# Kernel optimization log

Measured on AMD Instinct MI355X. Metric: run time of the kernel, lower is better.

Reference implementation:

```python
import jax, jax.numpy as jnp
import numpy as np

DECAY = 0.8      # cfg.ema_decay
EPS = 1e-5       # cfg.eps


def setup_inputs() -> dict:
    key = jax.random.key(0)
    k1, k2 = jax.random.split(key)
    H, B, N, D = 8, 8, 2048, 64   # num_codebooks, batch, seq, code_dim
    C = 1024                      # num_codes
    x = jax.random.normal(k1, (H, B, N, D), dtype=jnp.float32)
    embed = jax.random.normal(k2, (H, C, D), dtype=jnp.float32)
    embed_avg = embed.copy()
    cluster_size = jnp.ones((H, C), dtype=jnp.float32)
    return {"x": x, "embed": embed, "embed_avg": embed_avg, "cluster_size": cluster_size}


def reference(x, embed, embed_avg, cluster_size):
    # x: [h, b, n, d], embed: [h, c, d]
    h, b, n, d = x.shape
    c = embed.shape[1]
    flatten = x.reshape(h, b * n, d)  # pack 'h * d'

    # negative squared euclidean distance: -||f - e||^2
    f_sq = jnp.sum(flatten * flatten, axis=-1, keepdims=True)          # [h, N, 1]
    e_sq = jnp.sum(embed * embed, axis=-1)[:, None, :]                  # [h, 1, c]
    cross = jnp.einsum('hnd,hcd->hnc', flatten, embed)                  # [h, N, c]
    dist = -(f_sq - 2.0 * cross + e_sq)                                 # [h, N, c]

    # gumbel_sample with stochastic=False, straight_through=False -> argmax + one_hot
    embed_ind_flat = jnp.argmax(dist, axis=-1)                          # [h, N]
    embed_onehot = jax.nn.one_hot(embed_ind_flat, c, dtype=x.dtype)     # [h, N, c]

    # quantize (training path): onehot @ embed
    quantize = jnp.einsum('hnc,hcd->hnd', embed_onehot, embed).reshape(h, b, n, d)
    embed_ind = embed_ind_flat.reshape(h, b, n)

    # EMA codebook updates (ema_update=True, affine_params=False)
    cs_new = cluster_size * DECAY + embed_onehot.sum(axis=1) * (1.0 - DECAY)      # [h, c]
    embed_sum = jnp.einsum('hnd,hnc->hcd', flatten, embed_onehot)                  # [h, c, d]
    ea_new = embed_avg * DECAY + embed_sum * (1.0 - DECAY)                         # [h, c, d]

    ntot = jnp.sum(cs_new, axis=-1, keepdims=True)                                 # [h, 1]
    cs_smooth = (cs_new + EPS) / (ntot + c * EPS) * ntot                           # laplace smoothing * n
    embed_norm = ea_new / cs_smooth[..., None]                                     # new embed

    dist_out = dist.reshape(h, b, n, c)
    return quantize, embed_ind, embed_onehot, dist_out, embed_norm, ea_new, cs_new
```

## Files before the change

### kernel.cpp

```cpp
#include <hip/hip_runtime.h>

#define DECAY 0.8f
#define EPS   1e-5f
#define HN    8
#define BB    8
#define NSEQ  2048
#define DD    64
#define CC    1024
#define NROW  (BB*NSEQ)

#define LS 128
#define XS(k,r) xs[(k)*LS + (r)]
#define ES(k,c) es[(k)*LS + (c)]

typedef float vf4 __attribute__((ext_vector_type(4)));

__global__ void sumsq_kernel(const float* __restrict__ x, const float* __restrict__ embed,
                             float* __restrict__ fsq, float* __restrict__ esq) {
    int tid = blockIdx.x * blockDim.x + threadIdx.x;
    const int totalF = HN * NROW;
    const int totalE = HN * CC;
    if (tid < totalF) {
        const float4* src = (const float4*)(x + (size_t)tid * DD);
        float s = 0.f;
        #pragma unroll
        for (int i = 0; i < DD/4; ++i) {
            float4 v = src[i];
            s = fmaf(v.x, v.x, s); s = fmaf(v.y, v.y, s);
            s = fmaf(v.z, v.z, s); s = fmaf(v.w, v.w, s);
        }
        fsq[tid] = s;
    } else if (tid < totalF + totalE) {
        int t = tid - totalF;
        const float4* src = (const float4*)(embed + (size_t)t * DD);
        float s = 0.f;
        #pragma unroll
        for (int i = 0; i < DD/4; ++i) {
            float4 v = src[i];
            s = fmaf(v.x, v.x, s); s = fmaf(v.y, v.y, s);
            s = fmaf(v.z, v.z, s); s = fmaf(v.w, v.w, s);
        }
        esq[t] = s;
    }
}

__global__ __launch_bounds__(256, 2)
void dist_fp32_kernel(const float* __restrict__ x, const float* __restrict__ embed,
                      const float* __restrict__ fsq, const float* __restrict__ esq,
                      float* __restrict__ out_q, float* __restrict__ out_i,
                      float* __restrict__ out_oh, float* __restrict__ out_d) {
    __shared__ float xs[64 * LS];
    __shared__ float es[64 * LS];

    const int h   = blockIdx.y;
    const int n0  = blockIdx.x * 128;
    const int tid = threadIdx.x;
    const int ty  = tid >> 4;
    const int tx  = tid & 15;

    const float* xh_   = x     + (size_t)h * NROW * DD;
    const float* eh_   = embed + (size_t)h * CC   * DD;
    const float* esq_h = esq   + h * CC;

    const int g4 = (tid & 31) * 4;
    const int k0 = (tid >> 5) * 8;

    {
        float4 v[2][4];
        #pragma unroll
        for (int t = 0; t < 2; ++t)
            #pragma unroll
            for (int i = 0; i < 4; ++i)
                v[t][i] = *(const float4*)(xh_ + (size_t)(n0 + g4 + i) * DD + k0 + t*4);
        #pragma unroll
        for (int t = 0; t < 2; ++t) {
            *(float4*)&XS(k0+t*4+0, g4) = make_float4(v[t][0].x, v[t][1].x, v[t][2].x, v[t][3].x);
            *(float4*)&XS(k0+t*4+1, g4) = make_float4(v[t][0].y, v[t][1].y, v[t][2].y, v[t][3].y);
            *(float4*)&XS(k0+t*4+2, g4) = make_float4(v[t][0].z, v[t][1].z, v[t][2].z, v[t][3].z);
            *(float4*)&XS(k0+t*4+3, g4) = make_float4(v[t][0].w, v[t][1].w, v[t][2].w, v[t][3].w);
        }
    }
    {
        float4 v[2][4];
        #pragma unroll
        for (int t = 0; t < 2; ++t)
            #pragma unroll
            for (int i = 0; i < 4; ++i)
                v[t][i] = *(const float4*)(eh_ + (size_t)(g4 + i) * DD + k0 + t*4);
        #pragma unroll
        for (int t = 0; t < 2; ++t) {
            *(float4*)&ES(k0+t*4+0, g4) = make_float4(v[t][0].x, v[t][1].x, v[t][2].x, v[t][3].x);
            *(float4*)&ES(k0+t*4+1, g4) = make_float4(v[t][0].y, v[t][1].y, v[t][2].y, v[t][3].y);
            *(float4*)&ES(k0+t*4+2, g4) = make_float4(v[t][0].z, v[t][1].z, v[t][2].z, v[t][3].z);
            *(float4*)&ES(k0+t*4+3, g4) = make_float4(v[t][0].w, v[t][1].w, v[t][2].w, v[t][3].w);
        }
    }
    asm volatile("s_waitcnt lgkmcnt(0)" ::: "memory");
    __builtin_amdgcn_s_barrier();

    float fs[8];
    #pragma unroll
    for (int i = 0; i < 8; ++i) fs[i] = fsq[h*NROW + n0 + ty*8 + i];

    float bestv[8];
    int   besti[8];
    #pragma unroll
    for (int i = 0; i < 8; ++i) { bestv[i] = -3.4e38f; besti[i] = 0; }

    #pragma unroll 1
    for (int ci = 0; ci < 8; ++ci) {
        const int c0 = ci * 128;

        float4 ev[2][4];
        if (ci < 7) {
            #pragma unroll
            for (int t = 0; t < 2; ++t)
                #pragma unroll
                for (int i = 0; i < 4; ++i)
                    ev[t][i] = *(const float4*)(eh_ + (size_t)(c0 + 128 + g4 + i) * DD + k0 + t*4);
        }

        float acc[8][8];
        #pragma unroll
        for (int i = 0; i < 8; ++i)
            #pragma unroll
            for (int j = 0; j < 8; ++j) acc[i][j] = 0.f;

        #pragma unroll 4
        for (int k = 0; k < 64; ++k) {
            float a[8], b[8];
            *(float4*)&a[0] = *(const float4*)&XS(k, ty*8);
            *(float4*)&a[4] = *(const float4*)&XS(k, ty*8 + 4);
            *(float4*)&b[0] = *(const float4*)&ES(k, tx*4);
            *(float4*)&b[4] = *(const float4*)&ES(k, 64 + tx*4);
            #pragma unroll
            for (int i = 0; i < 8; ++i)
                #pragma unroll
                for (int j = 0; j < 8; ++j)
                    acc[i][j] = fmaf(a[i], b[j], acc[i][j]);
        }

        float eq[8];
        *(float4*)&eq[0] = *(const float4*)(esq_h + c0 + tx*4);
        *(float4*)&eq[4] = *(const float4*)(esq_h + c0 + 64 + tx*4);

        #pragma unroll
        for (int i = 0; i < 8; ++i) {
            int row = n0 + ty*8 + i;
            float dv[8];
            #pragma unroll
            for (int j = 0; j < 8; ++j)
                dv[j] = fmaf(2.f, acc[i][j], -(fs[i] + eq[j]));

            size_t rb = ((size_t)h*NROW + row)*CC + c0;
            vf4 d0 = {dv[0], dv[1], dv[2], dv[3]};
            vf4 d1 = {dv[4], dv[5], dv[6], dv[7]};
            __builtin_nontemporal_store(d0, (vf4*)(out_d + rb + tx*4));
            __builtin_nontemporal_store(d1, (vf4*)(out_d + rb + 64 + tx*4));

            #pragma unroll
            for (int j = 0; j < 4; ++j) {
                if (dv[j] > bestv[i]) { bestv[i] = dv[j]; besti[i] = c0 + tx*4 + j; }
            }
            #pragma unroll
            for (int j = 4; j < 8; ++j) {
                if (dv[j] > bestv[i]) { bestv[i] = dv[j]; besti[i] = c0 + 64 + tx*4 + (j-4); }
            }
        }

        if (ci < 7) {
            asm volatile("s_waitcnt lgkmcnt(0)" ::: "memory");
            __builtin_amdgcn_s_barrier();
            #pragma unroll
            for (int t = 0; t < 2; ++t) {
                *(float4*)&ES(k0+t*4+0, g4) = make_float4(ev[t][0].x, ev[t][1].x, ev[t][2].x, ev[t][3].x);
                *(float4*)&ES(k0+t*4+1, g4) = make_float4(ev[t][0].y, ev[t][1].y, ev[t][2].y, ev[t][3].y);
                *(float4*)&ES(k0+t*4+2, g4) = make_float4(ev[t][0].z, ev[t][1].z, ev[t][2].z, ev[t][3].z);
                *(float4*)&ES(k0+t*4+3, g4) = make_float4(ev[t][0].w, ev[t][1].w, ev[t][2].w, ev[t][3].w);
            }
            asm volatile("s_waitcnt lgkmcnt(0)" ::: "memory");
            __builtin_amdgcn_s_barrier();
        }
    }


    #pragma unroll
    for (int i = 0; i < 8; ++i) {
        float v  = bestv[i];
        int   id = besti[i];
        #pragma unroll
        for (int off = 8; off >= 1; off >>= 1) {
            float ov = __shfl_xor(v, off, 64);
            int   oi = __shfl_xor(id, off, 64);
            if (ov > v || (ov == v && oi < id)) { v = ov; id = oi; }
        }
        int row = n0 + ty*8 + i;
        float4 qv = *(const float4*)(eh_ + (size_t)id*DD + tx*4);
        *(float4*)(out_q + ((size_t)h*NROW + row)*DD + tx*4) = qv;
        if (tx == 0) {
            out_i[(size_t)h*NROW + row] = (float)id;
            out_oh[((size_t)h*NROW + row)*CC + id] = 1.0f;
        }
    }
}

__global__ __launch_bounds__(64)
void ema_kernel(const float* __restrict__ x, const float* __restrict__ embed_avg,
                const float* __restrict__ cluster_size, const float* __restrict__ ind_f,
                float* __restrict__ out_cs, float* __restrict__ out_ea,
                float* __restrict__ out_norm) {
    const int h    = blockIdx.y;
    const int c    = blockIdx.x;
    const int lane = threadIdx.x;

    const float* cs_h = cluster_size + h*CC;
    float s = 0.f;
    #pragma unroll
    for (int i = 0; i < CC/64; ++i) s += cs_h[lane + i*64];
    #pragma unroll
    for (int off = 32; off >= 1; off >>= 1) s += __shfl_xor(s, off, 64);

    const float* xh   = x     + (size_t)h * NROW * DD;
    const float* indh = ind_f + (size_t)h * NROW;

    float sum_d = 0.f;
    int   cnt   = 0;
    for (int chunk = 0; chunk < NROW/64; ++chunk) {
        int myidx = (int)indh[chunk*64 + lane];
        unsigned long long m = __ballot(myidx == c);
        while (m) {
            int t = __ffsll(m) - 1;
            m &= m - 1;
            int n = chunk*64 + t;
            sum_d += xh[(size_t)n*DD + lane];
            cnt++;
        }
    }

    float csn  = cs_h[c]*DECAY + (float)cnt*(1.f - DECAY);
    float ea   = embed_avg[((size_t)h*CC + c)*DD + lane]*DECAY + sum_d*(1.f - DECAY);
    float ntot = s*DECAY + (1.f - DECAY)*(float)NROW;
    float css  = (csn + EPS) / (ntot + (float)CC*EPS) * ntot;

    out_ea  [((size_t)h*CC + c)*DD + lane] = ea;
    out_norm[((size_t)h*CC + c)*DD + lane] = ea / css;
    if (lane == 0) out_cs[h*CC + c] = csn;
}

extern "C" void kernel_launch(void* const* d_in, const int* in_sizes, int n_in,
                              void* d_out, int out_size, void* d_ws, size_t ws_size,
                              hipStream_t stream) {
    const float* x            = (const float*)d_in[0];
    const float* embed        = (const float*)d_in[1];
    const float* embed_avg    = (const float*)d_in[2];
    const float* cluster_size = (const float*)d_in[3];

    float* out = (float*)d_out;
    float* fsq = (float*)d_ws;
    float* esq = fsq + (size_t)HN * NROW;

    float* out_q    = out;
    float* out_i    = out_q    + (size_t)HN * NROW * DD;
    float* out_oh   = out_i    + (size_t)HN * NROW;
    float* out_d    = out_oh   + (size_t)HN * NROW * CC;
    float* out_norm = out_d    + (size_t)HN * NROW * CC;
    float* out_ea   = out_norm + (size_t)HN * CC * DD;
    float* out_cs   = out_ea   + (size_t)HN * CC * DD;

    hipMemsetAsync(out_oh, 0, (size_t)HN * NROW * CC * sizeof(float), stream);

    {
        int total = HN*NROW + HN*CC;
        sumsq_kernel<<<(total + 255)/256, 256, 0, stream>>>(x, embed, fsq, esq);
    }
    {
        dim3 g(NROW/128, HN);
        dist_fp32_kernel<<<g, 256, 0, stream>>>(x, embed, fsq, esq,
                                                out_q, out_i, out_oh, out_d);
    }
    {
        dim3 g(CC, HN);
        ema_kernel<<<g, 64, 0, stream>>>(x, embed_avg, cluster_size, out_i,
                                         out_cs, out_ea, out_norm);
    }
}
```

Baseline: 540.8 us.

## Halve embed LDS tile into K-halves to fit three blocks per CU

The embed shared-memory tile is split into two 32-deep K halves that are streamed in sequence, which halves the LDS footprint and cuts the prefetch registers from eight float4 to four. Launch bounds are raised from 2 to 3 blocks per SM so more blocks can be resident to hide the heavy distance-matrix store traffic. The cost is twice as many barriers per codebook chunk and a tighter register budget, which could cause spills with the 64-entry accumulator.

```diff
diff --git a/kernel.cpp b/kernel.cpp
--- a/kernel.cpp
+++ b/kernel.cpp
@@ -15,6 +15,9 @@
 
 typedef float vf4 __attribute__((ext_vector_type(4)));
 
+#define LGKM0_BAR() do { asm volatile("s_waitcnt lgkmcnt(0)" ::: "memory"); \
+                         __builtin_amdgcn_s_barrier(); } while (0)
+
 __global__ void sumsq_kernel(const float* __restrict__ x, const float* __restrict__ embed,
                              float* __restrict__ fsq, float* __restrict__ esq) {
     int tid = blockIdx.x * blockDim.x + threadIdx.x;
@@ -44,13 +47,13 @@
     }
 }
 
-__global__ __launch_bounds__(256, 2)
+__global__ __launch_bounds__(256, 3)
 void dist_fp32_kernel(const float* __restrict__ x, const float* __restrict__ embed,
                       const float* __restrict__ fsq, const float* __restrict__ esq,
                       float* __restrict__ out_q, float* __restrict__ out_i,
                       float* __restrict__ out_oh, float* __restrict__ out_d) {
     __shared__ float xs[64 * LS];
-    __shared__ float es[64 * LS];
+    __shared__ float es[32 * LS];
 
     const int h   = blockIdx.y;
     const int n0  = blockIdx.x * 128;
@@ -62,8 +65,9 @@
     const float* eh_   = embed + (size_t)h * CC   * DD;
     const float* esq_h = esq   + h * CC;
 
-    const int g4 = (tid & 31) * 4;
-    const int k0 = (tid >> 5) * 8;
+    const int g4  = (tid & 31) * 4;
+    const int k0x = (tid >> 5) * 8;
+    const int k0  = (tid >> 5) * 4;
 
     {
         float4 v[2][4];
@@ -71,32 +75,22 @@
         for (int t = 0; t < 2; ++t)
             #pragma unroll
             for (int i = 0; i < 4; ++i)
-                v[t][i] = *(const float4*)(xh_ + (size_t)(n0 + g4 + i) * DD + k0 + t*4);
+                v[t][i] = *(const float4*)(xh_ + (size_t)(n0 + g4 + i) * DD + k0x + t*4);
         #pragma unroll
         for (int t = 0; t < 2; ++t) {
-            *(float4*)&XS(k0+t*4+0, g4) = make_float4(v[t][0].x, v[t][1].x, v[t][2].x, v[t][3].x);
-            *(float4*)&XS(k0+t*4+1, g4) = make_float4(v[t][0].y, v[t][1].y, v[t][2].y, v[t][3].y);
-            *(float4*)&XS(k0+t*4+2, g4) = make_float4(v[t][0].z, v[t][1].z, v[t][2].z, v[t][3].z);
-            *(float4*)&XS(k0+t*4+3, g4) = make_float4(v[t][0].w, v[t][1].w, v[t][2].w, v[t][3].w);
-        }
-    }
-    {
-        float4 v[2][4];
-        #pragma unroll
-        for (int t = 0; t < 2; ++t)
-            #pragma unroll
-            for (int i = 0; i < 4; ++i)
-                v[t][i] = *(const float4*)(eh_ + (size_t)(g4 + i) * DD + k0 + t*4);
-        #pragma unroll
-        for (int t = 0; t < 2; ++t) {
-            *(float4*)&ES(k0+t*4+0, g4) = make_float4(v[t][0].x, v[t][1].x, v[t][2].x, v[t][3].x);
-            *(float4*)&ES(k0+t*4+1, g4) = make_float4(v[t][0].y, v[t][1].y, v[t][2].y, v[t][3].y);
-            *(float4*)&ES(k0+t*4+2, g4) = make_float4(v[t][0].z, v[t][1].z, v[t][2].z, v[t][3].z);
-            *(float4*)&ES(k0+t*4+3, g4) = make_float4(v[t][0].w, v[t][1].w, v[t][2].w, v[t][3].w);
-        }
-    }
-    asm volatile("s_waitcnt lgkmcnt(0)" ::: "memory");
-    __builtin_amdgcn_s_barrier();
+            *(float4*)&XS(k0x+t*4+0, g4) = make_float4(v[t][0].x, v[t][1].x, v[t][2].x, v[t][3].x);
+            *(float4*)&XS(k0x+t*4+1, g4) = make_float4(v[t][0].y, v[t][1].y, v[t][2].y, v[t][3].y);
+            *(float4*)&XS(k0x+t*4+2, g4) = make_float4(v[t][0].z, v[t][1].z, v[t][2].z, v[t][3].z);
+            *(float4*)&XS(k0x+t*4+3, g4) = make_float4(v[t][0].w, v[t][1].w, v[t][2].w, v[t][3].w);
+        }
+    }
+
+    float4 ev[4];
+    #pragma unroll
+    for (int i = 0; i < 4; ++i)
+        ev[i] = *(const float4*)(eh_ + (size_t)(g4 + i) * DD + k0);
+
+    LGKM0_BAR();
 
     float fs[8];
     #pragma unroll
@@ -107,30 +101,42 @@
     #pragma unroll
     for (int i = 0; i < 8; ++i) { bestv[i] = -3.4e38f; besti[i] = 0; }
 
+    float acc[8][8];
+
     #pragma unroll 1
-    for (int ci = 0; ci < 8; ++ci) {
-        const int c0 = ci * 128;
-
-        float4 ev[2][4];
-        if (ci < 7) {
-            #pragma unroll
-            for (int t = 0; t < 2; ++t)
-                #pragma unroll
-                for (int i = 0; i < 4; ++i)
-                    ev[t][i] = *(const float4*)(eh_ + (size_t)(c0 + 128 + g4 + i) * DD + k0 + t*4);
-        }
-
-        float acc[8][8];
-        #pragma unroll
-        for (int i = 0; i < 8; ++i)
-            #pragma unroll
-            for (int j = 0; j < 8; ++j) acc[i][j] = 0.f;
-
+    for (int p = 0; p < 16; ++p) {
+        const int kh = p & 1;
+        const int c0 = (p >> 1) * 128;
+
+        *(float4*)&ES(k0+0, g4) = make_float4(ev[0].x, ev[1].x, ev[2].x, ev[3].x);
+        *(float4*)&ES(k0+1, g4) = make_float4(ev[0].y, ev[1].y, ev[2].y, ev[3].y);
+        *(float4*)&ES(k0+2, g4) = make_float4(ev[0].z, ev[1].z, ev[2].z, ev[3].z);
+        *(float4*)&ES(k0+3, g4) = make_float4(ev[0].w, ev[1].w, ev[2].w, ev[3].w);
+
+        if (p < 15) {
+            const int pn  = p + 1;
+            const int c0n = (pn >> 1) * 128;
+            const int khn = (pn & 1) * 32;
+            #pragma unroll
+            for (int i = 0; i < 4; ++i)
+                ev[i] = *(const float4*)(eh_ + (size_t)(c0n + g4 + i) * DD + khn + k0);
+        }
+
+        LGKM0_BAR();
+
+        if (kh == 0) {
+            #pragma unroll
+            for (int i = 0; i < 8; ++i)
+                #pragma unroll
+                for (int j = 0; j < 8; ++j) acc[i][j] = 0.f;
+        }
+
+        const float* xsb = &XS(kh*32, 0);
         #pragma unroll 4
-        for (int k = 0; k < 64; ++k) {
+        for (int k = 0; k < 32; ++k) {
             float a[8], b[8];
-            *(float4*)&a[0] = *(const float4*)&XS(k, ty*8);
-            *(float4*)&a[4] = *(const float4*)&XS(k, ty*8 + 4);
+            *(float4*)&a[0] = *(const float4*)&xsb[k*LS + ty*8];
+            *(float4*)&a[4] = *(const float4*)&xsb[k*LS + ty*8 + 4];
             *(float4*)&b[0] = *(const float4*)&ES(k, tx*4);
             *(float4*)&b[4] = *(const float4*)&ES(k, 64 + tx*4);
             #pragma unroll
@@ -140,49 +146,38 @@
                     acc[i][j] = fmaf(a[i], b[j], acc[i][j]);
         }
 
-        float eq[8];
-        *(float4*)&eq[0] = *(const float4*)(esq_h + c0 + tx*4);
-        *(float4*)&eq[4] = *(const float4*)(esq_h + c0 + 64 + tx*4);
-
-        #pragma unroll
-        for (int i = 0; i < 8; ++i) {
-            int row = n0 + ty*8 + i;
-            float dv[8];
-            #pragma unroll
-            for (int j = 0; j < 8; ++j)
-                dv[j] = fmaf(2.f, acc[i][j], -(fs[i] + eq[j]));
-
-            size_t rb = ((size_t)h*NROW + row)*CC + c0;
-            vf4 d0 = {dv[0], dv[1], dv[2], dv[3]};
-            vf4 d1 = {dv[4], dv[5], dv[6], dv[7]};
-            __builtin_nontemporal_store(d0, (vf4*)(out_d + rb + tx*4));
-            __builtin_nontemporal_store(d1, (vf4*)(out_d + rb + 64 + tx*4));
-
-            #pragma unroll
-            for (int j = 0; j < 4; ++j) {
-                if (dv[j] > bestv[i]) { bestv[i] = dv[j]; besti[i] = c0 + tx*4 + j; }
+        if (kh == 1) {
+            float eq[8];
+            *(float4*)&eq[0] = *(const float4*)(esq_h + c0 + tx*4);
+            *(float4*)&eq[4] = *(const float4*)(esq_h + c0 + 64 + tx*4);
+
+            #pragma unroll
+            for (int i = 0; i < 8; ++i) {
+                int row = n0 + ty*8 + i;
+                float dv[8];
+                #pragma unroll
+                for (int j = 0; j < 8; ++j)
+                    dv[j] = fmaf(2.f, acc[i][j], -(fs[i] + eq[j]));
+
+                size_t rb = ((size_t)h*NROW + row)*CC + c0;
+                vf4 d0 = {dv[0], dv[1], dv[2], dv[3]};
+                vf4 d1 = {dv[4], dv[5], dv[6], dv[7]};
+                __builtin_nontemporal_store(d0, (vf4*)(out_d + rb + tx*4));
+                __builtin_nontemporal_store(d1, (vf4*)(out_d + rb + 64 + tx*4));
+
+                #pragma unroll
+                for (int j = 0; j < 4; ++j) {
+                    if (dv[j] > bestv[i]) { bestv[i] = dv[j]; besti[i] = c0 + tx*4 + j; }
+                }
+                #pragma unroll
+                for (int j = 4; j < 8; ++j) {
+                    if (dv[j] > bestv[i]) { bestv[i] = dv[j]; besti[i] = c0 + 64 + tx*4 + (j-4); }
+                }
             }
-            #pragma unroll
-            for (int j = 4; j < 8; ++j) {
-                if (dv[j] > bestv[i]) { bestv[i] = dv[j]; besti[i] = c0 + 64 + tx*4 + (j-4); }
-            }
-        }
-
-        if (ci < 7) {
-            asm volatile("s_waitcnt lgkmcnt(0)" ::: "memory");
-            __builtin_amdgcn_s_barrier();
-            #pragma unroll
-            for (int t = 0; t < 2; ++t) {
-                *(float4*)&ES(k0+t*4+0, g4) = make_float4(ev[t][0].x, ev[t][1].x, ev[t][2].x, ev[t][3].x);
-                *(float4*)&ES(k0+t*4+1, g4) = make_float4(ev[t][0].y, ev[t][1].y, ev[t][2].y, ev[t][3].y);
-                *(float4*)&ES(k0+t*4+2, g4) = make_float4(ev[t][0].z, ev[t][1].z, ev[t][2].z, ev[t][3].z);
-                *(float4*)&ES(k0+t*4+3, g4) = make_float4(ev[t][0].w, ev[t][1].w, ev[t][2].w, ev[t][3].w);
-            }
-            asm volatile("s_waitcnt lgkmcnt(0)" ::: "memory");
-            __builtin_amdgcn_s_barrier();
-        }
-    }
-
+        }
+
+        LGKM0_BAR();
+    }
 
     #pragma unroll
     for (int i = 0; i < 8; ++i) {
```

After: 706.6 us. 30.7% more time.

## Compute distances with split-fp16 MFMA and fix near-tie argmax in fp32

Applied to the files above, without the earlier changes.

Replaces the fp32 FMA distance GEMM with MFMA 16x16x32 fp16 instructions. Each operand is split into hi and lo fp16 parts and three products are accumulated to approximate fp32 precision. The kernel tracks the top-two distances per row and writes a margin. Rows whose margin is below a threshold are recomputed exactly in fp32 by a new fixup kernel, and a finalize kernel writes quantize and the one-hot. The aim is to cut ALU time on the GEMM, at the cost of extra launches, slightly less exact dist values, and stores that are now scalar rather than vectorized.

```diff
diff --git a/kernel.cpp b/kernel.cpp
--- a/kernel.cpp
+++ b/kernel.cpp
@@ -8,12 +8,16 @@
 #define DD    64
 #define CC    1024
 #define NROW  (BB*NSEQ)
-
-#define LS 128
-#define XS(k,r) xs[(k)*LS + (r)]
-#define ES(k,c) es[(k)*LS + (c)]
-
-typedef float vf4 __attribute__((ext_vector_type(4)));
+#define TAU   0.1f
+
+typedef _Float16 f16x8 __attribute__((ext_vector_type(8)));
+typedef float    f32x4 __attribute__((ext_vector_type(4)));
+
+#define MFMA16(a,b,c) __builtin_amdgcn_mfma_f32_16x16x32_f16(a, b, c, 0, 0, 0)
+
+#define BAR() do { asm volatile("s_waitcnt lgkmcnt(0)" ::: "memory"); \
+                   __builtin_amdgcn_s_barrier(); \
+                   asm volatile("" ::: "memory"); } while (0)
 
 __global__ void sumsq_kernel(const float* __restrict__ x, const float* __restrict__ embed,
                              float* __restrict__ fsq, float* __restrict__ esq) {
@@ -44,164 +48,240 @@
     }
 }
 
+__device__ __forceinline__ void cvt8(const float* vv, f16x8* hi, f16x8* lo) {
+    f16x8 h, l;
+    #pragma unroll
+    for (int j = 0; j < 8; ++j) {
+        _Float16 hh = (_Float16)vv[j];
+        h[j] = hh;
+        l[j] = (_Float16)(vv[j] - (float)hh);
+    }
+    *hi = h; *lo = l;
+}
+
+__device__ __forceinline__ int lds_off(int col, int k) {
+    return (col * 128 + k * 2) ^ ((col & 7) << 4);
+}
+
 __global__ __launch_bounds__(256, 2)
-void dist_fp32_kernel(const float* __restrict__ x, const float* __restrict__ embed,
+void dist_mfma_kernel(const float* __restrict__ x, const float* __restrict__ embed,
                       const float* __restrict__ fsq, const float* __restrict__ esq,
-                      float* __restrict__ out_q, float* __restrict__ out_i,
-                      float* __restrict__ out_oh, float* __restrict__ out_d) {
-    __shared__ float xs[64 * LS];
-    __shared__ float es[64 * LS];
+                      float* __restrict__ out_i, float* __restrict__ margin,
+                      float* __restrict__ out_d) {
+    __shared__ _Float16 eb[2][2][128 * 64];
 
     const int h   = blockIdx.y;
     const int n0  = blockIdx.x * 128;
     const int tid = threadIdx.x;
-    const int ty  = tid >> 4;
-    const int tx  = tid & 15;
+    const int wv  = tid >> 6;
+    const int l   = tid & 63;
+    const int l15 = l & 15;
+    const int l4  = l >> 4;
 
     const float* xh_   = x     + (size_t)h * NROW * DD;
     const float* eh_   = embed + (size_t)h * CC   * DD;
     const float* esq_h = esq   + h * CC;
 
-    const int g4 = (tid & 31) * 4;
-    const int k0 = (tid >> 5) * 8;
-
-    {
-        float4 v[2][4];
-        #pragma unroll
-        for (int t = 0; t < 2; ++t)
-            #pragma unroll
-            for (int i = 0; i < 4; ++i)
-                v[t][i] = *(const float4*)(xh_ + (size_t)(n0 + g4 + i) * DD + k0 + t*4);
-        #pragma unroll
-        for (int t = 0; t < 2; ++t) {
-            *(float4*)&XS(k0+t*4+0, g4) = make_float4(v[t][0].x, v[t][1].x, v[t][2].x, v[t][3].x);
-            *(float4*)&XS(k0+t*4+1, g4) = make_float4(v[t][0].y, v[t][1].y, v[t][2].y, v[t][3].y);
-            *(float4*)&XS(k0+t*4+2, g4) = make_float4(v[t][0].z, v[t][1].z, v[t][2].z, v[t][3].z);
-            *(float4*)&XS(k0+t*4+3, g4) = make_float4(v[t][0].w, v[t][1].w, v[t][2].w, v[t][3].w);
-        }
-    }
-    {
-        float4 v[2][4];
-        #pragma unroll
-        for (int t = 0; t < 2; ++t)
-            #pragma unroll
-            for (int i = 0; i < 4; ++i)
-                v[t][i] = *(const float4*)(eh_ + (size_t)(g4 + i) * DD + k0 + t*4);
-        #pragma unroll
-        for (int t = 0; t < 2; ++t) {
-            *(float4*)&ES(k0+t*4+0, g4) = make_float4(v[t][0].x, v[t][1].x, v[t][2].x, v[t][3].x);
-            *(float4*)&ES(k0+t*4+1, g4) = make_float4(v[t][0].y, v[t][1].y, v[t][2].y, v[t][3].y);
-            *(float4*)&ES(k0+t*4+2, g4) = make_float4(v[t][0].z, v[t][1].z, v[t][2].z, v[t][3].z);
-            *(float4*)&ES(k0+t*4+3, g4) = make_float4(v[t][0].w, v[t][1].w, v[t][2].w, v[t][3].w);
-        }
-    }
-    asm volatile("s_waitcnt lgkmcnt(0)" ::: "memory");
-    __builtin_amdgcn_s_barrier();
-
-    float fs[8];
-    #pragma unroll
-    for (int i = 0; i < 8; ++i) fs[i] = fsq[h*NROW + n0 + ty*8 + i];
-
-    float bestv[8];
-    int   besti[8];
-    #pragma unroll
-    for (int i = 0; i < 8; ++i) { bestv[i] = -3.4e38f; besti[i] = 0; }
+    f16x8 Ah[2][2], Al[2][2];
+    #pragma unroll
+    for (int rt = 0; rt < 2; ++rt)
+        #pragma unroll
+        for (int ks = 0; ks < 2; ++ks) {
+            const float* src = xh_ + (size_t)(n0 + wv*32 + rt*16 + l15) * DD + ks*32 + l4*8;
+            float4 v0 = *(const float4*)src;
+            float4 v1 = *(const float4*)(src + 4);
+            float vv[8] = {v0.x, v0.y, v0.z, v0.w, v1.x, v1.y, v1.z, v1.w};
+            cvt8(vv, &Ah[rt][ks], &Al[rt][ks]);
+        }
+
+    float fs[2][4];
+    #pragma unroll
+    for (int rt = 0; rt < 2; ++rt)
+        #pragma unroll
+        for (int r = 0; r < 4; ++r)
+            fs[rt][r] = fsq[h*NROW + n0 + wv*32 + rt*16 + l4*4 + r];
+
+    const int scol = tid >> 1;
+    const int sk0  = (tid & 1) * 32;
+    {
+        const float* src = eh_ + (size_t)scol * DD + sk0;
+        float arr[32];
+        #pragma unroll
+        for (int i = 0; i < 8; ++i) {
+            float4 v = *(const float4*)(src + 4*i);
+            arr[4*i+0] = v.x; arr[4*i+1] = v.y; arr[4*i+2] = v.z; arr[4*i+3] = v.w;
+        }
+        #pragma unroll
+        for (int g = 0; g < 4; ++g) {
+            f16x8 hi, lo;
+            cvt8(&arr[8*g], &hi, &lo);
+            int off = lds_off(scol, sk0 + 8*g);
+            *(f16x8*)((char*)&eb[0][0][0] + off) = hi;
+            *(f16x8*)((char*)&eb[0][1][0] + off) = lo;
+        }
+    }
+    BAR();
+
+    float best1[2][4], best2[2][4];
+    int   bid[2][4];
+    #pragma unroll
+    for (int rt = 0; rt < 2; ++rt)
+        #pragma unroll
+        for (int r = 0; r < 4; ++r) {
+            best1[rt][r] = -3.4e38f; best2[rt][r] = -3.4e38f; bid[rt][r] = 0;
+        }
 
     #pragma unroll 1
     for (int ci = 0; ci < 8; ++ci) {
         const int c0 = ci * 128;
-
-        float4 ev[2][4];
+        const int b  = ci & 1;
+
+        float arr[32];
         if (ci < 7) {
-            #pragma unroll
-            for (int t = 0; t < 2; ++t)
+            const float* src = eh_ + (size_t)(c0 + 128 + scol) * DD + sk0;
+            #pragma unroll
+            for (int i = 0; i < 8; ++i) {
+                float4 v = *(const float4*)(src + 4*i);
+                arr[4*i+0] = v.x; arr[4*i+1] = v.y; arr[4*i+2] = v.z; arr[4*i+3] = v.w;
+            }
+        }
+
+        const _Float16* ph = &eb[b][0][0];
+        const _Float16* pl = &eb[b][1][0];
+
+        #pragma unroll
+        for (int ct = 0; ct < 8; ++ct) {
+            const int col  = ct*16 + l15;
+            const int colg = c0 + col;
+            f16x8 Bh0 = *(const f16x8*)((const char*)ph + lds_off(col, 0  + l4*8));
+            f16x8 Bh1 = *(const f16x8*)((const char*)ph + lds_off(col, 32 + l4*8));
+            f16x8 Bl0 = *(const f16x8*)((const char*)pl + lds_off(col, 0  + l4*8));
+            f16x8 Bl1 = *(const f16x8*)((const char*)pl + lds_off(col, 32 + l4*8));
+
+            f32x4 a0 = {0.f, 0.f, 0.f, 0.f};
+            f32x4 a1 = {0.f, 0.f, 0.f, 0.f};
+            a0 = MFMA16(Ah[0][0], Bh0, a0); a1 = MFMA16(Ah[1][0], Bh0, a1);
+            a0 = MFMA16(Ah[0][1], Bh1, a0); a1 = MFMA16(Ah[1][1], Bh1, a1);
+            a0 = MFMA16(Ah[0][0], Bl0, a0); a1 = MFMA16(Ah[1][0], Bl0, a1);
+            a0 = MFMA16(Ah[0][1], Bl1, a0); a1 = MFMA16(Ah[1][1], Bl1, a1);
+            a0 = MFMA16(Al[0][0], Bh0, a0); a1 = MFMA16(Al[1][0], Bh0, a1);
+            a0 = MFMA16(Al[0][1], Bh1, a0); a1 = MFMA16(Al[1][1], Bh1, a1);
+
+            const float eq = esq_h[colg];
+            #pragma unroll
+            for (int rt = 0; rt < 2; ++rt) {
+                const f32x4 acc = rt ? a1 : a0;
                 #pragma unroll
-                for (int i = 0; i < 4; ++i)
-                    ev[t][i] = *(const float4*)(eh_ + (size_t)(c0 + 128 + g4 + i) * DD + k0 + t*4);
-        }
-
-        float acc[8][8];
-        #pragma unroll
-        for (int i = 0; i < 8; ++i)
-            #pragma unroll
-            for (int j = 0; j < 8; ++j) acc[i][j] = 0.f;
-
-        #pragma unroll 4
-        for (int k = 0; k < 64; ++k) {
-            float a[8], b[8];
-            *(float4*)&a[0] = *(const float4*)&XS(k, ty*8);
-            *(float4*)&a[4] = *(const float4*)&XS(k, ty*8 + 4);
-            *(float4*)&b[0] = *(const float4*)&ES(k, tx*4);
-            *(float4*)&b[4] = *(const float4*)&ES(k, 64 + tx*4);
-            #pragma unroll
-            for (int i = 0; i < 8; ++i)
-                #pragma unroll
-                for (int j = 0; j < 8; ++j)
-                    acc[i][j] = fmaf(a[i], b[j], acc[i][j]);
-        }
-
-        float eq[8];
-        *(float4*)&eq[0] = *(const float4*)(esq_h + c0 + tx*4);
-        *(float4*)&eq[4] = *(const float4*)(esq_h + c0 + 64 + tx*4);
-
-        #pragma unroll
-        for (int i = 0; i < 8; ++i) {
-            int row = n0 + ty*8 + i;
-            float dv[8];
-            #pragma unroll
-            for (int j = 0; j < 8; ++j)
-                dv[j] = fmaf(2.f, acc[i][j], -(fs[i] + eq[j]));
-
-            size_t rb = ((size_t)h*NROW + row)*CC + c0;
-            vf4 d0 = {dv[0], dv[1], dv[2], dv[3]};
-            vf4 d1 = {dv[4], dv[5], dv[6], dv[7]};
-            __builtin_nontemporal_store(d0, (vf4*)(out_d + rb + tx*4));
-            __builtin_nontemporal_store(d1, (vf4*)(out_d + rb + 64 + tx*4));
-
-            #pragma unroll
-            for (int j = 0; j < 4; ++j) {
-                if (dv[j] > bestv[i]) { bestv[i] = dv[j]; besti[i] = c0 + tx*4 + j; }
-            }
-            #pragma unroll
-            for (int j = 4; j < 8; ++j) {
-                if (dv[j] > bestv[i]) { bestv[i] = dv[j]; besti[i] = c0 + 64 + tx*4 + (j-4); }
+                for (int r = 0; r < 4; ++r) {
+                    float dv = fmaf(2.f, acc[r], -(fs[rt][r] + eq));
+                    int row = n0 + wv*32 + rt*16 + l4*4 + r;
+                    __builtin_nontemporal_store(dv, out_d + ((size_t)h*NROW + row)*CC + colg);
+                    if (dv > best1[rt][r]) {
+                        best2[rt][r] = best1[rt][r];
+                        best1[rt][r] = dv;
+                        bid[rt][r]   = colg;
+                    } else if (dv > best2[rt][r]) {
+                        best2[rt][r] = dv;
+                    }
+                }
             }
         }
 
         if (ci < 7) {
-            asm volatile("s_waitcnt lgkmcnt(0)" ::: "memory");
-            __builtin_amdgcn_s_barrier();
-            #pragma unroll
-            for (int t = 0; t < 2; ++t) {
-                *(float4*)&ES(k0+t*4+0, g4) = make_float4(ev[t][0].x, ev[t][1].x, ev[t][2].x, ev[t][3].x);
-                *(float4*)&ES(k0+t*4+1, g4) = make_float4(ev[t][0].y, ev[t][1].y, ev[t][2].y, ev[t][3].y);
-                *(float4*)&ES(k0+t*4+2, g4) = make_float4(ev[t][0].z, ev[t][1].z, ev[t][2].z, ev[t][3].z);
-                *(float4*)&ES(k0+t*4+3, g4) = make_float4(ev[t][0].w, ev[t][1].w, ev[t][2].w, ev[t][3].w);
-            }
-            asm volatile("s_waitcnt lgkmcnt(0)" ::: "memory");
-            __builtin_amdgcn_s_barrier();
-        }
-    }
-
-
-    #pragma unroll
-    for (int i = 0; i < 8; ++i) {
-        float v  = bestv[i];
-        int   id = besti[i];
-        #pragma unroll
-        for (int off = 8; off >= 1; off >>= 1) {
-            float ov = __shfl_xor(v, off, 64);
-            int   oi = __shfl_xor(id, off, 64);
-            if (ov > v || (ov == v && oi < id)) { v = ov; id = oi; }
-        }
-        int row = n0 + ty*8 + i;
-        float4 qv = *(const float4*)(eh_ + (size_t)id*DD + tx*4);
-        *(float4*)(out_q + ((size_t)h*NROW + row)*DD + tx*4) = qv;
-        if (tx == 0) {
-            out_i[(size_t)h*NROW + row] = (float)id;
-            out_oh[((size_t)h*NROW + row)*CC + id] = 1.0f;
-        }
-    }
+            #pragma unroll
+            for (int g = 0; g < 4; ++g) {
+                f16x8 hi, lo;
+                cvt8(&arr[8*g], &hi, &lo);
+                int off = lds_off(scol, sk0 + 8*g);
+                *(f16x8*)((char*)&eb[b^1][0][0] + off) = hi;
+                *(f16x8*)((char*)&eb[b^1][1][0] + off) = lo;
+            }
+        }
+        BAR();
+    }
+
+    #pragma unroll
+    for (int rt = 0; rt < 2; ++rt) {
+        #pragma unroll
+        for (int r = 0; r < 4; ++r) {
+            float v1 = best1[rt][r], v2 = best2[rt][r];
+            int   id = bid[rt][r];
+            #pragma unroll
+            for (int off = 8; off >= 1; off >>= 1) {
+                float ov = __shfl_xor(v1, off, 64);
+                int   oi = __shfl_xor(id, off, 64);
+                float ow = __shfl_xor(v2, off, 64);
+                float lo = (ov > v1) ? v1 : ov;
+                if (ov > v1 || (ov == v1 && oi < id)) { v1 = ov; id = oi; }
+                v2 = fmaxf(fmaxf(v2, ow), lo);
+            }
+            if (l15 == 0) {
+                int row = n0 + wv*32 + rt*16 + l4*4 + r;
+                out_i [(size_t)h*NROW + row] = (float)id;
+                margin[(size_t)h*NROW + row] = v1 - v2;
+            }
+        }
+    }
+}
+
+__global__ __launch_bounds__(64)
+void fixup_kernel(const float* __restrict__ x, const float* __restrict__ embed,
+                  const float* __restrict__ fsq, const float* __restrict__ esq,
+                  const float* __restrict__ margin, float* __restrict__ out_i) {
+    const int blk  = blockIdx.x;
+    const int h    = blk >> 8;
+    const int r0   = (blk & 255) * 64;
+    const int lane = threadIdx.x;
+
+    float m = margin[(size_t)h*NROW + r0 + lane];
+    unsigned long long mask = __ballot(m < TAU);
+
+    while (mask) {
+        int t = __ffsll(mask) - 1;
+        mask &= mask - 1;
+        const int row = r0 + t;
+
+        const float* xr  = x + ((size_t)h*NROW + row)*DD;
+        const float  fsv = fsq[(size_t)h*NROW + row];
+
+        float best = -3.4e38f;
+        int   bidx = 0;
+        for (int g = 0; g < 16; ++g) {
+            const int c = g*64 + lane;
+            const float* er = embed + ((size_t)h*CC + c)*DD;
+            float acc = 0.f;
+            #pragma unroll
+            for (int k4 = 0; k4 < 16; ++k4) {
+                float4 xv = *(const float4*)(xr + k4*4);
+                float4 ev = *(const float4*)(er + k4*4);
+                acc = fmaf(xv.x, ev.x, acc); acc = fmaf(xv.y, ev.y, acc);
+                acc = fmaf(xv.z, ev.z, acc); acc = fmaf(xv.w, ev.w, acc);
+            }
+            float dv = fmaf(2.f, acc, -(fsv + esq[h*CC + c]));
+            if (dv > best) { best = dv; bidx = c; }
+        }
+        #pragma unroll
+        for (int off = 32; off >= 1; off >>= 1) {
+            float ov = __shfl_xor(best, off, 64);
+            int   oi = __shfl_xor(bidx, off, 64);
+            if (ov > best || (ov == best && oi < bidx)) { best = ov; bidx = oi; }
+        }
+        if (lane == 0) out_i[(size_t)h*NROW + row] = (float)bidx;
+    }
+}
+
+__global__ __launch_bounds__(256)
+void finalize_kernel(const float* __restrict__ embed, const float* __restrict__ out_i,
+                     float* __restrict__ out_q, float* __restrict__ out_oh) {
+    const int t   = blockIdx.x * 256 + threadIdx.x;
+    const int row = t >> 4;
+    const int lx  = t & 15;
+    const int id  = (int)out_i[row];
+    const int h   = row >> 14;
+
+    float4 qv = *(const float4*)(embed + ((size_t)h*CC + id)*DD + lx*4);
+    *(float4*)(out_q + (size_t)row*DD + lx*4) = qv;
+    if (lx == 0) out_oh[(size_t)row*CC + id] = 1.0f;
 }
 
 __global__ __launch_bounds__(64)
@@ -256,8 +336,9 @@
     const float* cluster_size = (const float*)d_in[3];
 
     float* out = (float*)d_out;
-    float* fsq = (float*)d_ws;
-    float* esq = fsq + (size_t)HN * NROW;
+    float* fsq    = (float*)d_ws;
+    float* esq    = fsq    + (size_t)HN * NROW;
+    float* margin = esq    + (size_t)HN * CC;
 
     float* out_q    = out;
     float* out_i    = out_q    + (size_t)HN * NROW * DD;
@@ -275,8 +356,14 @@
     }
     {
         dim3 g(NROW/128, HN);
-        dist_fp32_kernel<<<g, 256, 0, stream>>>(x, embed, fsq, esq,
-                                                out_q, out_i, out_oh, out_d);
+        dist_mfma_kernel<<<g, 256, 0, stream>>>(x, embed, fsq, esq,
+                                                out_i, margin, out_d);
+    }
+    {
+        fixup_kernel<<<HN * (NROW/64), 64, 0, stream>>>(x, embed, fsq, esq, margin, out_i);
+    }
+    {
+        finalize_kernel<<<(HN*NROW*16)/256, 256, 0, stream>>>(embed, out_i, out_q, out_oh);
     }
     {
         dim3 g(CC, HN);
```

New measurement: 715.1 us, median of 2. 1.32x slower.
